# Performance work log

Hardware: AMD Instinct MI355X
Metric: run time of the kernel (lower is better)

Reference implementation:

```python
import jax, jax.numpy as jnp
import numpy as np

N_AE = 512
N_DE = 256
N = 100000
NUM_SEG = 1024
EPS = 1e-5


def setup_inputs() -> dict:
    key = jax.random.key(0)
    ks = jax.random.split(key, 20)
    d_in1 = 2 * N_AE + N_DE  # 1280
    inp = {
        "x": jax.random.normal(ks[0], (N, 2 * N_AE), dtype=jnp.float32),
        "dist_feat": jax.random.normal(ks[1], (N, N_DE), dtype=jnp.float32),
        "atom_idx": jax.random.randint(ks[2], (N,), 0, 100, dtype=jnp.int32),
        "ele_idx": jax.random.randint(ks[3], (N,), 0, NUM_SEG, dtype=jnp.int32),
        # layer 1 params
        "l1_w": jax.random.normal(ks[4], (d_in1, N_AE), dtype=jnp.float32) * (1.0 / np.sqrt(d_in1)),
        "l1_b": jnp.zeros((N_AE,), dtype=jnp.float32),
        "l1_g": jnp.ones((N_AE,), dtype=jnp.float32),
        "l1_be": jnp.zeros((N_AE,), dtype=jnp.float32),
        # layer 2 params (same input width: 2*n_ae + n_de)
        "l2_w": jax.random.normal(ks[5], (d_in1, N_AE), dtype=jnp.float32) * (1.0 / np.sqrt(d_in1)),
        "l2_b": jnp.zeros((N_AE,), dtype=jnp.float32),
        "l2_g": jnp.ones((N_AE,), dtype=jnp.float32),
        "l2_be": jnp.zeros((N_AE,), dtype=jnp.float32),
        # final fc + bn
        "f_w": jax.random.normal(ks[6], (2 * N_AE, N_AE), dtype=jnp.float32) * (1.0 / np.sqrt(2 * N_AE)),
        "f_b": jnp.zeros((N_AE,), dtype=jnp.float32),
        "f_g": jnp.ones((N_AE,), dtype=jnp.float32),
        "f_be": jnp.zeros((N_AE,), dtype=jnp.float32),
    }
    return inp


def _bn(h, gamma, beta):
    # BatchNorm1d in training mode: batch stats, biased variance
    m = jnp.mean(h, axis=0)
    v = jnp.mean(jnp.square(h - m), axis=0)
    return gamma * (h - m) * jax.lax.rsqrt(v + EPS) + beta


def _dist_layer(x_cat, ele_idx, w, b, gamma, beta):
    h = jax.nn.relu(_bn(x_cat @ w + b, gamma, beta))  # [N, n_ae]
    sums = jax.ops.segment_sum(h, ele_idx, num_segments=NUM_SEG)  # [S, n_ae]
    cnt = jax.ops.segment_sum(jnp.ones((h.shape[0],), h.dtype), ele_idx, num_segments=NUM_SEG)
    mean = sums / jnp.maximum(cnt, 1.0)[:, None]
    return jnp.concatenate([h, mean[ele_idx]], axis=1)  # [N, 2*n_ae]


def reference(x, dist_feat, atom_idx, ele_idx,
              l1_w, l1_b, l1_g, l1_be,
              l2_w, l2_b, l2_g, l2_be,
              f_w, f_b, f_g, f_be):
    h = _dist_layer(jnp.concatenate([x, dist_feat], axis=1), ele_idx, l1_w, l1_b, l1_g, l1_be)
    h = _dist_layer(jnp.concatenate([h, dist_feat], axis=1), ele_idx, l2_w, l2_b, l2_g, l2_be)
    out = jax.nn.relu(_bn(h @ f_w + f_b, f_g, f_be))  # [N, n_ae]
    return out
```

## Files before the change

kernel.cpp:

```cpp
#include <hip/hip_runtime.h>
#include <stdint.h>
#include <stdio.h>

#define NOUT 512
#define NSEG 1024

typedef unsigned short u16;
typedef __attribute__((ext_vector_type(4))) float f32x4;
typedef __attribute__((ext_vector_type(8))) short s16x8;
typedef __attribute__((ext_vector_type(4))) unsigned short u16x4;

__device__ __forceinline__ u16 f2b(float f) {
  union { float f; uint32_t u; } v; v.f = f;
  uint32_t r = v.u + 0x7FFFu + ((v.u >> 16) & 1u);
  return (u16)(r >> 16);
}
__device__ __forceinline__ float b2f(u16 b) {
  union { uint32_t u; float f; } v; v.u = ((uint32_t)b) << 16;
  return v.f;
}

typedef __attribute__((address_space(1))) const void GAS;
typedef __attribute__((address_space(3))) void LAS;
__device__ __forceinline__ void llds16(const void* g, void* l) {
  __builtin_amdgcn_global_load_lds((GAS*)g, (LAS*)l, 16, 0, 0);
}

__global__ void k_cast(const float* __restrict__ src, u16* __restrict__ dst, long n4) {
  long i = blockIdx.x * (long)blockDim.x + threadIdx.x;
  long stride = (long)gridDim.x * blockDim.x;
  for (; i < n4; i += stride) {
    float4 v = reinterpret_cast<const float4*>(src)[i];
    u16x4 o;
    o.x = f2b(v.x); o.y = f2b(v.y); o.z = f2b(v.z); o.w = f2b(v.w);
    reinterpret_cast<u16x4*>(dst)[i] = o;
  }
}

__global__ void k_wtcastT(const float* __restrict__ w, u16* __restrict__ out, int K) {
  __shared__ float tile[32][33];
  int k0 = blockIdx.x * 32, c0 = blockIdx.y * 32;
  int t = threadIdx.x;
  int rr = t >> 5, cc = t & 31;
#pragma unroll
  for (int p = 0; p < 4; ++p)
    tile[p * 8 + rr][cc] = w[(long)(k0 + p * 8 + rr) * NOUT + c0 + cc];
  __syncthreads();
#pragma unroll
  for (int p = 0; p < 4; ++p)
    out[(long)(c0 + p * 8 + rr) * K + k0 + cc] = f2b(tile[cc][p * 8 + rr]);
}

__global__ void k_hist(const int* __restrict__ ele, int* __restrict__ cnt, int N) {
  int i = blockIdx.x * blockDim.x + threadIdx.x;
  int stride = gridDim.x * blockDim.x;
  for (; i < N; i += stride) atomicAdd(&cnt[ele[i]], 1);
}

__global__ void k_scan(const int* __restrict__ cnt, int* __restrict__ off) {
  __shared__ int tmp[NSEG];
  int t = threadIdx.x;
  tmp[t] = cnt[t];
  __syncthreads();
  for (int o = 1; o < NSEG; o <<= 1) {
    int add = (t >= o) ? tmp[t - o] : 0;
    __syncthreads();
    tmp[t] += add;
    __syncthreads();
  }
  off[t] = tmp[t] - cnt[t];
}

__global__ void k_scatter(const int* __restrict__ ele, const int* __restrict__ off,
                          int* __restrict__ fill, int* __restrict__ rows, int N) {
  int i = blockIdx.x * blockDim.x + threadIdx.x;
  int stride = gridDim.x * blockDim.x;
  for (; i < N; i += stride) {
    int e = ele[i];
    int p = atomicAdd(&fill[e], 1);
    rows[off[e] + p] = i;
  }
}

__global__ void k_colreduce(const float* __restrict__ ps, const float* __restrict__ pq,
                            float* __restrict__ sum, float* __restrict__ sq, int rows) {
  int gid = blockIdx.x * blockDim.x + threadIdx.x;
  int col = gid & 511;
  int arr = (gid >> 9) & 1;
  int chunk = gid >> 10;
  const float* src = arr ? pq : ps;
  float acc = 0.f;
  for (int r = chunk; r < rows; r += 16) acc += src[(long)r * NOUT + col];
  atomicAdd(arr ? &sq[col] : &sum[col], acc);
}

__global__ void k_finalize(const float* __restrict__ sum, const float* __restrict__ sumsq,
                           const float* __restrict__ g, const float* __restrict__ be,
                           float* __restrict__ A, float* __restrict__ C, int M) {
  int c = threadIdx.x;
  float m = sum[c] / (float)M;
  float v = sumsq[c] / (float)M - m * m;
  float a = g[c] * rsqrtf(v + 1e-5f);
  A[c] = a;
  C[c] = be[c] - a * m;
}

__global__ void k_bnseg(const u16* __restrict__ hp, u16* __restrict__ h, u16* __restrict__ mean,
                        const float* __restrict__ A, const float* __restrict__ C,
                        const int* __restrict__ off, const int* __restrict__ cnt,
                        const int* __restrict__ rows) {
  int s = blockIdx.x;
  int c0 = blockIdx.y * 256 + 2 * threadIdx.x;
  int n = cnt[s], o = off[s];
  float a0 = A[c0], a1 = A[c0 + 1], cc0 = C[c0], cc1 = C[c0 + 1];
  float s0 = 0.f, s1 = 0.f;
  for (int j = 0; j < n; ++j) {
    int r = rows[o + j];
    uint32_t v = *reinterpret_cast<const uint32_t*>(&hp[(long)r * NOUT + c0]);
    float h0 = fmaxf(a0 * b2f((u16)(v & 0xffff)) + cc0, 0.f);
    float h1 = fmaxf(a1 * b2f((u16)(v >> 16)) + cc1, 0.f);
    s0 += h0; s1 += h1;
    *reinterpret_cast<uint32_t*>(&h[(long)r * NOUT + c0]) =
        ((uint32_t)f2b(h1) << 16) | (uint32_t)f2b(h0);
  }
  float inv = 1.f / fmaxf((float)n, 1.f);
  *reinterpret_cast<uint32_t*>(&mean[(long)s * NOUT + c0]) =
      ((uint32_t)f2b(s1 * inv) << 16) | (uint32_t)f2b(s0 * inv);
}

__global__ void k_final(const u16* __restrict__ hp, float* __restrict__ out,
                        const float* __restrict__ A, const float* __restrict__ C, long n4) {
  long i = blockIdx.x * (long)blockDim.x + threadIdx.x;
  long stride = (long)gridDim.x * blockDim.x;
  for (; i < n4; i += stride) {
    u16x4 v = reinterpret_cast<const u16x4*>(hp)[i];
    int c0 = (int)((i * 4) & (NOUT - 1));
    float4 a = *reinterpret_cast<const float4*>(&A[c0]);
    float4 c = *reinterpret_cast<const float4*>(&C[c0]);
    float4 o;
    o.x = fmaxf(a.x * b2f(v.x) + c.x, 0.f);
    o.y = fmaxf(a.y * b2f(v.y) + c.y, 0.f);
    o.z = fmaxf(a.z * b2f(v.z) + c.z, 0.f);
    o.w = fmaxf(a.w * b2f(v.w) + c.w, 0.f);
    reinterpret_cast<float4*>(out)[i] = o;
  }
}

__global__ __launch_bounds__(256, 2) void k_gemm(
    const u16* p0, const u16* p1, int e0, int w0, int w1, int g0, int g1,
    const int* __restrict__ ele,
    const u16* __restrict__ wbt, int ldb, int e0b, int bskip,
    const float* __restrict__ tab, int addtab,
    u16* __restrict__ outp, float* __restrict__ outf, int wf32,
    float* __restrict__ ps, float* __restrict__ pq, int dostats,
    int M, int K) {
  __shared__ __align__(16) u16 As[128 * 32];
  __shared__ __align__(16) u16 Bs[128 * 32];

  int nwg = gridDim.x;
  int bid = blockIdx.x;
  if ((nwg & 7) == 0) {
    int chunk = nwg >> 3;
    bid = (bid & 7) * chunk + (bid >> 3);
  }
  int mt = bid >> 2, ct = bid & 3;
  int brow = mt * 128, bcol = ct * 128;

  int tid = (int)threadIdx.x;
  int lane = tid & 63;
  int wv = tid >> 6;
  int wr = wv >> 1, wc = wv & 1;
  int l4 = lane >> 2;
  int c8 = lane & 3;
  int socl = (c8 ^ ((l4 >> 1) & 3)) * 8;

  int rr0 = brow + wv * 32 + l4;
  int r0 = rr0 < M ? rr0 : M - 1;
  int rr1 = rr0 + 16;
  int r1 = rr1 < M ? rr1 : M - 1;
  int el0 = ele[r0], el1 = ele[r1];

  const u16* a00 = p0 + (long)(g0 ? el0 : r0) * w0 + socl;
  const u16* a01 = p1 + (long)(g1 ? el0 : r0) * w1 + socl - e0;
  const u16* a10 = p0 + (long)(g0 ? el1 : r1) * w0 + socl;
  const u16* a11 = p1 + (long)(g1 ? el1 : r1) * w1 + socl - e0;

  int cb = bcol + wv * 32 + l4;
  const u16* b0p = wbt + (long)cb * ldb + socl;
  const u16* b1p = b0p + (long)16 * ldb;

  u16* ldsA0 = &As[wv * 1024];
  u16* ldsA1 = ldsA0 + 512;
  u16* ldsB0 = &Bs[wv * 1024];
  u16* ldsB1 = ldsB0 + 512;

  f32x4 acc[4][4];
#pragma unroll
  for (int m = 0; m < 4; ++m)
#pragma unroll
    for (int n = 0; n < 4; ++n)
#pragma unroll
      for (int j = 0; j < 4; ++j) acc[m][n][j] = 0.f;

  int l15 = lane & 15, kg = lane >> 4;
  int axr = (kg ^ ((l15 >> 1) & 3)) * 8;
  int KT = K >> 5;
  for (int ks = 0; ks < KT; ++ks) {
    int k0 = ks << 5;
    const u16* sa0 = k0 < e0 ? a00 : a01;
    const u16* sa1 = k0 < e0 ? a10 : a11;
    int bo = k0 + (k0 >= e0b ? bskip : 0);
    __syncthreads();
    llds16(sa0 + k0, ldsA0);
    llds16(sa1 + k0, ldsA1);
    llds16(b0p + bo, ldsB0);
    llds16(b1p + bo, ldsB1);
    __syncthreads();
    s16x8 af[4], bf[4];
#pragma unroll
    for (int m = 0; m < 4; ++m)
      af[m] = *reinterpret_cast<const s16x8*>(&As[(wr * 64 + m * 16 + l15) * 32 + axr]);
#pragma unroll
    for (int n = 0; n < 4; ++n)
      bf[n] = *reinterpret_cast<const s16x8*>(&Bs[(wc * 64 + n * 16 + l15) * 32 + axr]);
#pragma unroll
    for (int m = 0; m < 4; ++m)
#pragma unroll
      for (int n = 0; n < 4; ++n)
        acc[m][n] = __builtin_amdgcn_mfma_f32_16x16x32_bf16(af[m], bf[n], acc[m][n], 0, 0, 0);
  }

  float sums[4] = {0.f, 0.f, 0.f, 0.f}, sqs[4] = {0.f, 0.f, 0.f, 0.f};
#pragma unroll
  for (int m = 0; m < 4; ++m) {
    int row0 = brow + wr * 64 + m * 16 + kg * 4;
#pragma unroll
    for (int n = 0; n < 4; ++n) {
      int col = bcol + wc * 64 + n * 16 + l15;
#pragma unroll
      for (int j = 0; j < 4; ++j) {
        int r = row0 + j;
        if (r < M) {
          float v = acc[m][n][j];
          if (addtab) v += tab[(long)ele[r] * NOUT + col];
          if (wf32) outf[(long)r * NOUT + col] = v;
          else outp[(long)r * NOUT + col] = f2b(v);
          sums[n] += v;
          sqs[n] += v * v;
        }
      }
    }
  }
  if (dostats) {
#pragma unroll
    for (int n = 0; n < 4; ++n) {
      sums[n] += __shfl_xor(sums[n], 16);
      sums[n] += __shfl_xor(sums[n], 32);
      sqs[n] += __shfl_xor(sqs[n], 16);
      sqs[n] += __shfl_xor(sqs[n], 32);
    }
    if (kg == 0) {
      long prow = (long)(mt * 2 + wr) * NOUT;
#pragma unroll
      for (int n = 0; n < 4; ++n) {
        int col = bcol + wc * 64 + n * 16 + l15;
        ps[prow + col] = sums[n];
        pq[prow + col] = sqs[n];
      }
    }
  }
}

extern "C" void kernel_launch(void* const* d_in, const int* in_sizes, int n_in,
                              void* d_out, int out_size, void* d_ws, size_t ws_size,
                              hipStream_t stream) {
  const float* x    = (const float*)d_in[0];
  const float* dist = (const float*)d_in[1];
  const int* ele    = (const int*)d_in[3];
  const float* l1w  = (const float*)d_in[4];
  const float* l1g  = (const float*)d_in[6];
  const float* l1be = (const float*)d_in[7];
  const float* l2w  = (const float*)d_in[8];
  const float* l2g  = (const float*)d_in[10];
  const float* l2be = (const float*)d_in[11];
  const float* fw   = (const float*)d_in[12];
  const float* fg   = (const float*)d_in[14];
  const float* fbe  = (const float*)d_in[15];

  int N = in_sizes[0] / 1024;
  float* out = (float*)d_out;
  u16* xbf = (u16*)d_out;

  int MT = (N + 127) / 128;
  int prows = MT * 2;

  char* w = (char*)d_ws;
  auto alloc = [&](size_t bytes) {
    char* p = w;
    w += (bytes + 255) & ~(size_t)255;
    return p;
  };
  u16* dist_bf = (u16*)alloc((size_t)N * 256 * 2);
  u16* hp      = (u16*)alloc((size_t)N * NOUT * 2);
  u16* h       = (u16*)alloc((size_t)N * NOUT * 2);
  u16* mean    = (u16*)alloc((size_t)NSEG * NOUT * 2);
  u16* w1bt    = (u16*)alloc((size_t)NOUT * 1280 * 2);
  u16* w2bt    = (u16*)alloc((size_t)NOUT * 1280 * 2);
  u16* fbt     = (u16*)alloc((size_t)NOUT * 1024 * 2);
  float* mc2   = (float*)alloc((size_t)NSEG * NOUT * 4);
  float* mc3   = (float*)alloc((size_t)NSEG * NOUT * 4);
  float* ps    = (float*)alloc((size_t)prows * NOUT * 4);
  float* pq    = (float*)alloc((size_t)prows * NOUT * 4);
  float* colsum = (float*)alloc(NOUT * 4 * 2);
  float* colsumsq = colsum + NOUT;
  float* bnA   = (float*)alloc(NOUT * 4);
  float* bnC   = (float*)alloc(NOUT * 4);
  int* seg_cnt = (int*)alloc(NSEG * 4);
  int* seg_off = (int*)alloc(NSEG * 4);
  int* seg_fill = (int*)alloc(NSEG * 4);
  int* rows    = (int*)alloc((size_t)N * 4);

  size_t need = (size_t)(w - (char*)d_ws);
  if (need > ws_size) {
    fprintf(stderr, "kernel_launch: ws too small: need %zu have %zu\n", need, ws_size);
    return;
  }

  long n4x = (long)N * 1024 / 4;
  long n4d = (long)N * 256 / 4;
  long n4h = (long)N * NOUT / 4;
  int gemmGrid = MT * 4;
  int mcGrid = (NSEG / 128) * 4;
  dim3 bnsegGrid(NSEG, 2);

  k_cast<<<4096, 256, 0, stream>>>(x, xbf, n4x);
  k_cast<<<2048, 256, 0, stream>>>(dist, dist_bf, n4d);
  dim3 wt1(1280 / 32, 16), wt3(1024 / 32, 16);
  k_wtcastT<<<wt1, 256, 0, stream>>>(l1w, w1bt, 1280);
  k_wtcastT<<<wt1, 256, 0, stream>>>(l2w, w2bt, 1280);
  k_wtcastT<<<wt3, 256, 0, stream>>>(fw, fbt, 1024);

  hipMemsetAsync(seg_cnt, 0, NSEG * 4, stream);
  hipMemsetAsync(seg_fill, 0, NSEG * 4, stream);
  k_hist<<<512, 256, 0, stream>>>(ele, seg_cnt, N);
  k_scan<<<1, NSEG, 0, stream>>>(seg_cnt, seg_off);
  k_scatter<<<512, 256, 0, stream>>>(ele, seg_off, seg_fill, rows, N);

  k_gemm<<<gemmGrid, 256, 0, stream>>>(xbf, dist_bf, 1024, 1024, 256, 0, 0, ele,
                                       w1bt, 1280, 1280, 0, mc2, 0,
                                       hp, mc2, 0, ps, pq, 1, N, 1280);
  hipMemsetAsync(colsum, 0, NOUT * 4 * 2, stream);
  k_colreduce<<<64, 256, 0, stream>>>(ps, pq, colsum, colsumsq, prows);
  k_finalize<<<1, NOUT, 0, stream>>>(colsum, colsumsq, l1g, l1be, bnA, bnC, N);
  k_bnseg<<<bnsegGrid, 128, 0, stream>>>(hp, h, mean, bnA, bnC, seg_off, seg_cnt, rows);

  k_gemm<<<mcGrid, 256, 0, stream>>>(mean, mean, 512, 512, 512, 0, 0, ele,
                                     w2bt + 512, 1280, 512, 0, mc2, 0,
                                     hp, mc2, 1, ps, pq, 0, NSEG, 512);
  k_gemm<<<gemmGrid, 256, 0, stream>>>(h, dist_bf, 512, 512, 256, 0, 0, ele,
                                       w2bt, 1280, 512, 512, mc2, 1,
                                       hp, mc2, 0, ps, pq, 1, N, 768);
  hipMemsetAsync(colsum, 0, NOUT * 4 * 2, stream);
  k_colreduce<<<64, 256, 0, stream>>>(ps, pq, colsum, colsumsq, prows);
  k_finalize<<<1, NOUT, 0, stream>>>(colsum, colsumsq, l2g, l2be, bnA, bnC, N);
  k_bnseg<<<bnsegGrid, 128, 0, stream>>>(hp, h, mean, bnA, bnC, seg_off, seg_cnt, rows);

  k_gemm<<<mcGrid, 256, 0, stream>>>(mean, mean, 512, 512, 512, 0, 0, ele,
                                     fbt + 512, 1024, 512, 0, mc3, 0,
                                     hp, mc3, 1, ps, pq, 0, NSEG, 512);
  k_gemm<<<gemmGrid, 256, 0, stream>>>(h, h, 512, 512, 512, 0, 0, ele,
                                       fbt, 1024, 512, 0, mc3, 1,
                                       hp, mc3, 0, ps, pq, 1, N, 512);
  hipMemsetAsync(colsum, 0, NOUT * 4 * 2, stream);
  k_colreduce<<<64, 256, 0, stream>>>(ps, pq, colsum, colsumsq, prows);
  k_finalize<<<1, NOUT, 0, stream>>>(colsum, colsumsq, fg, fbe, bnA, bnC, N);
  k_final<<<4096, 256, 0, stream>>>(hp, out, bnA, bnC, n4h);
}
```

Measured before the change: 1.112 ms.

## Enlarge GEMM tile to 128x256xK64 and fuse BN column stats via atomics

The GEMM tile grows from 128x128 with K=32 to 128x256 with K=64, so each wave holds 4x8 MFMA accumulators. This raises operand reuse per LDS load and halves the number of barriers per K. The XCD block remapping is generalized to grids that are not a multiple of 8. Per-tile partial BN statistics are now atomically added straight into column sums, which drops the partial-sum buffers and the separate colreduce kernel. In exchange it uses more registers and LDS, which may lower occupancy, and it adds atomic contention and nondeterministic float summation order.

```diff
diff --git a/kernel.cpp b/kernel.cpp
--- a/kernel.cpp
+++ b/kernel.cpp
@@ -80,18 +80,6 @@
     int p = atomicAdd(&fill[e], 1);
     rows[off[e] + p] = i;
   }
-}
-
-__global__ void k_colreduce(const float* __restrict__ ps, const float* __restrict__ pq,
-                            float* __restrict__ sum, float* __restrict__ sq, int rows) {
-  int gid = blockIdx.x * blockDim.x + threadIdx.x;
-  int col = gid & 511;
-  int arr = (gid >> 9) & 1;
-  int chunk = gid >> 10;
-  const float* src = arr ? pq : ps;
-  float acc = 0.f;
-  for (int r = chunk; r < rows; r += 16) acc += src[(long)r * NOUT + col];
-  atomicAdd(arr ? &sq[col] : &sum[col], acc);
 }
 
 __global__ void k_finalize(const float* __restrict__ sum, const float* __restrict__ sumsq,
@@ -152,99 +140,111 @@
     const u16* __restrict__ wbt, int ldb, int e0b, int bskip,
     const float* __restrict__ tab, int addtab,
     u16* __restrict__ outp, float* __restrict__ outf, int wf32,
-    float* __restrict__ ps, float* __restrict__ pq, int dostats,
+    float* __restrict__ csum, float* __restrict__ csq, int dostats,
     int M, int K) {
-  __shared__ __align__(16) u16 As[128 * 32];
-  __shared__ __align__(16) u16 Bs[128 * 32];
+  __shared__ __align__(16) u16 As[128 * 64];
+  __shared__ __align__(16) u16 Bs[256 * 64];
 
   int nwg = gridDim.x;
-  int bid = blockIdx.x;
-  if ((nwg & 7) == 0) {
-    int chunk = nwg >> 3;
-    bid = (bid & 7) * chunk + (bid >> 3);
-  }
-  int mt = bid >> 2, ct = bid & 3;
-  int brow = mt * 128, bcol = ct * 128;
+  int orig = blockIdx.x;
+  int q = nwg >> 3, r8 = nwg & 7;
+  int xcd = orig & 7, loc = orig >> 3;
+  int bid = (xcd < r8 ? xcd * (q + 1) : r8 * (q + 1) + (xcd - r8) * q) + loc;
+  int mt = bid >> 1, ct = bid & 1;
+  int brow = mt * 128, bcol = ct * 256;
 
   int tid = (int)threadIdx.x;
   int lane = tid & 63;
-  int wv = tid >> 6;
-  int wr = wv >> 1, wc = wv & 1;
-  int l4 = lane >> 2;
-  int c8 = lane & 3;
-  int socl = (c8 ^ ((l4 >> 1) & 3)) * 8;
-
-  int rr0 = brow + wv * 32 + l4;
-  int r0 = rr0 < M ? rr0 : M - 1;
-  int rr1 = rr0 + 16;
-  int r1 = rr1 < M ? rr1 : M - 1;
-  int el0 = ele[r0], el1 = ele[r1];
-
-  const u16* a00 = p0 + (long)(g0 ? el0 : r0) * w0 + socl;
-  const u16* a01 = p1 + (long)(g1 ? el0 : r0) * w1 + socl - e0;
-  const u16* a10 = p0 + (long)(g0 ? el1 : r1) * w0 + socl;
-  const u16* a11 = p1 + (long)(g1 ? el1 : r1) * w1 + socl - e0;
-
-  int cb = bcol + wv * 32 + l4;
-  const u16* b0p = wbt + (long)cb * ldb + socl;
-  const u16* b1p = b0p + (long)16 * ldb;
-
-  u16* ldsA0 = &As[wv * 1024];
-  u16* ldsA1 = ldsA0 + 512;
-  u16* ldsB0 = &Bs[wv * 1024];
-  u16* ldsB1 = ldsB0 + 512;
-
-  f32x4 acc[4][4];
+  int wid = tid >> 6;
+  int wr = wid >> 1, wc = wid & 1;
+  int l15 = lane & 15, kg = lane >> 4;
+
+  int rl = tid >> 3;
+  int soct = ((tid & 7) ^ (rl & 7)) * 8;
+
+  int rida0[4], rida1[4];
+#pragma unroll
+  for (int c = 0; c < 4; ++c) {
+    int gr = brow + rl + 32 * c;
+    if (gr >= M) gr = M - 1;
+    int e = (g0 | g1) ? ele[gr] : 0;
+    rida0[c] = g0 ? e : gr;
+    rida1[c] = g1 ? e : gr;
+  }
+  const u16* bptr[8];
+#pragma unroll
+  for (int c = 0; c < 8; ++c)
+    bptr[c] = wbt + (long)(bcol + rl + 32 * c) * ldb + soct;
+
+  int ch0 = (kg ^ (l15 & 7)) * 8;
+  int ch1 = ((4 | kg) ^ (l15 & 7)) * 8;
+  int arow = (wr * 64 + l15) * 64;
+  int brow_l = (wc * 128 + l15) * 64;
+
+  f32x4 acc[4][8];
 #pragma unroll
   for (int m = 0; m < 4; ++m)
 #pragma unroll
-    for (int n = 0; n < 4; ++n)
+    for (int n = 0; n < 8; ++n)
 #pragma unroll
       for (int j = 0; j < 4; ++j) acc[m][n][j] = 0.f;
 
-  int l15 = lane & 15, kg = lane >> 4;
-  int axr = (kg ^ ((l15 >> 1) & 3)) * 8;
-  int KT = K >> 5;
-  for (int ks = 0; ks < KT; ++ks) {
-    int k0 = ks << 5;
-    const u16* sa0 = k0 < e0 ? a00 : a01;
-    const u16* sa1 = k0 < e0 ? a10 : a11;
+  int KT = K >> 6;
+  for (int t = 0; t < KT; ++t) {
+    int k0 = t << 6;
+    __syncthreads();
+    if (k0 < e0) {
+#pragma unroll
+      for (int c = 0; c < 4; ++c)
+        llds16(p0 + (long)rida0[c] * w0 + soct + k0, &As[c * 2048 + wid * 512]);
+    } else {
+      int ko = k0 - e0;
+#pragma unroll
+      for (int c = 0; c < 4; ++c)
+        llds16(p1 + (long)rida1[c] * w1 + soct + ko, &As[c * 2048 + wid * 512]);
+    }
     int bo = k0 + (k0 >= e0b ? bskip : 0);
+#pragma unroll
+    for (int c = 0; c < 8; ++c)
+      llds16(bptr[c] + bo, &Bs[c * 2048 + wid * 512]);
     __syncthreads();
-    llds16(sa0 + k0, ldsA0);
-    llds16(sa1 + k0, ldsA1);
-    llds16(b0p + bo, ldsB0);
-    llds16(b1p + bo, ldsB1);
-    __syncthreads();
-    s16x8 af[4], bf[4];
-#pragma unroll
-    for (int m = 0; m < 4; ++m)
-      af[m] = *reinterpret_cast<const s16x8*>(&As[(wr * 64 + m * 16 + l15) * 32 + axr]);
-#pragma unroll
-    for (int n = 0; n < 4; ++n)
-      bf[n] = *reinterpret_cast<const s16x8*>(&Bs[(wc * 64 + n * 16 + l15) * 32 + axr]);
-#pragma unroll
-    for (int m = 0; m < 4; ++m)
-#pragma unroll
-      for (int n = 0; n < 4; ++n)
-        acc[m][n] = __builtin_amdgcn_mfma_f32_16x16x32_bf16(af[m], bf[n], acc[m][n], 0, 0, 0);
-  }
-
-  float sums[4] = {0.f, 0.f, 0.f, 0.f}, sqs[4] = {0.f, 0.f, 0.f, 0.f};
+#pragma unroll
+    for (int kk = 0; kk < 2; ++kk) {
+      int ch = kk ? ch1 : ch0;
+      s16x8 af[4], bf[8];
+#pragma unroll
+      for (int m = 0; m < 4; ++m)
+        af[m] = *reinterpret_cast<const s16x8*>(&As[arow + m * 1024 + ch]);
+#pragma unroll
+      for (int n = 0; n < 8; ++n)
+        bf[n] = *reinterpret_cast<const s16x8*>(&Bs[brow_l + n * 1024 + ch]);
+#pragma unroll
+      for (int m = 0; m < 4; ++m)
+#pragma unroll
+        for (int n = 0; n < 8; ++n)
+          acc[m][n] = __builtin_amdgcn_mfma_f32_16x16x32_bf16(af[m], bf[n], acc[m][n], 0, 0, 0);
+    }
+  }
+
+  float sums[8], sqs[8];
+#pragma unroll
+  for (int n = 0; n < 8; ++n) { sums[n] = 0.f; sqs[n] = 0.f; }
 #pragma unroll
   for (int m = 0; m < 4; ++m) {
     int row0 = brow + wr * 64 + m * 16 + kg * 4;
 #pragma unroll
-    for (int n = 0; n < 4; ++n) {
-      int col = bcol + wc * 64 + n * 16 + l15;
-#pragma unroll
-      for (int j = 0; j < 4; ++j) {
-        int r = row0 + j;
-        if (r < M) {
+    for (int j = 0; j < 4; ++j) {
+      int r = row0 + j;
+      if (r < M) {
+        long rb = (long)r * NOUT;
+        long tb = addtab ? (long)ele[r] * NOUT : 0;
+#pragma unroll
+        for (int n = 0; n < 8; ++n) {
+          int col = bcol + wc * 128 + n * 16 + l15;
           float v = acc[m][n][j];
-          if (addtab) v += tab[(long)ele[r] * NOUT + col];
-          if (wf32) outf[(long)r * NOUT + col] = v;
-          else outp[(long)r * NOUT + col] = f2b(v);
+          if (addtab) v += tab[tb + col];
+          if (wf32) outf[rb + col] = v;
+          else outp[rb + col] = f2b(v);
           sums[n] += v;
           sqs[n] += v * v;
         }
@@ -253,19 +253,18 @@
   }
   if (dostats) {
 #pragma unroll
-    for (int n = 0; n < 4; ++n) {
+    for (int n = 0; n < 8; ++n) {
       sums[n] += __shfl_xor(sums[n], 16);
       sums[n] += __shfl_xor(sums[n], 32);
       sqs[n] += __shfl_xor(sqs[n], 16);
       sqs[n] += __shfl_xor(sqs[n], 32);
     }
     if (kg == 0) {
-      long prow = (long)(mt * 2 + wr) * NOUT;
-#pragma unroll
-      for (int n = 0; n < 4; ++n) {
-        int col = bcol + wc * 64 + n * 16 + l15;
-        ps[prow + col] = sums[n];
-        pq[prow + col] = sqs[n];
+#pragma unroll
+      for (int n = 0; n < 8; ++n) {
+        int col = bcol + wc * 128 + n * 16 + l15;
+        atomicAdd(&csum[col], sums[n]);
+        atomicAdd(&csq[col], sqs[n]);
       }
     }
   }
@@ -292,7 +291,6 @@
   u16* xbf = (u16*)d_out;
 
   int MT = (N + 127) / 128;
-  int prows = MT * 2;
 
   char* w = (char*)d_ws;
   auto alloc = [&](size_t bytes) {
@@ -309,8 +307,6 @@
   u16* fbt     = (u16*)alloc((size_t)NOUT * 1024 * 2);
   float* mc2   = (float*)alloc((size_t)NSEG * NOUT * 4);
   float* mc3   = (float*)alloc((size_t)NSEG * NOUT * 4);
-  float* ps    = (float*)alloc((size_t)prows * NOUT * 4);
-  float* pq    = (float*)alloc((size_t)prows * NOUT * 4);
   float* colsum = (float*)alloc(NOUT * 4 * 2);
   float* colsumsq = colsum + NOUT;
   float* bnA   = (float*)alloc(NOUT * 4);
@@ -329,8 +325,8 @@
   long n4x = (long)N * 1024 / 4;
   long n4d = (long)N * 256 / 4;
   long n4h = (long)N * NOUT / 4;
-  int gemmGrid = MT * 4;
-  int mcGrid = (NSEG / 128) * 4;
+  int gemmGrid = MT * 2;
+  int mcGrid = (NSEG / 128) * 2;
   dim3 bnsegGrid(NSEG, 2);
 
   k_cast<<<4096, 256, 0, stream>>>(x, xbf, n4x);
@@ -346,33 +342,30 @@
   k_scan<<<1, NSEG, 0, stream>>>(seg_cnt, seg_off);
   k_scatter<<<512, 256, 0, stream>>>(ele, seg_off, seg_fill, rows, N);
 
+  hipMemsetAsync(colsum, 0, NOUT * 4 * 2, stream);
   k_gemm<<<gemmGrid, 256, 0, stream>>>(xbf, dist_bf, 1024, 1024, 256, 0, 0, ele,
                                        w1bt, 1280, 1280, 0, mc2, 0,
-                                       hp, mc2, 0, ps, pq, 1, N, 1280);
-  hipMemsetAsync(colsum, 0, NOUT * 4 * 2, stream);
-  k_colreduce<<<64, 256, 0, stream>>>(ps, pq, colsum, colsumsq, prows);
+                                       hp, mc2, 0, colsum, colsumsq, 1, N, 1280);
   k_finalize<<<1, NOUT, 0, stream>>>(colsum, colsumsq, l1g, l1be, bnA, bnC, N);
   k_bnseg<<<bnsegGrid, 128, 0, stream>>>(hp, h, mean, bnA, bnC, seg_off, seg_cnt, rows);
 
   k_gemm<<<mcGrid, 256, 0, stream>>>(mean, mean, 512, 512, 512, 0, 0, ele,
                                      w2bt + 512, 1280, 512, 0, mc2, 0,
-                                     hp, mc2, 1, ps, pq, 0, NSEG, 512);
+                                     hp, mc2, 1, colsum, colsumsq, 0, NSEG, 512);
+  hipMemsetAsync(colsum, 0, NOUT * 4 * 2, stream);
   k_gemm<<<gemmGrid, 256, 0, stream>>>(h, dist_bf, 512, 512, 256, 0, 0, ele,
                                        w2bt, 1280, 512, 512, mc2, 1,
-                                       hp, mc2, 0, ps, pq, 1, N, 768);
-  hipMemsetAsync(colsum, 0, NOUT * 4 * 2, stream);
-  k_colreduce<<<64, 256, 0, stream>>>(ps, pq, colsum, colsumsq, prows);
+                                       hp, mc2, 0, colsum, colsumsq, 1, N, 768);
   k_finalize<<<1, NOUT, 0, stream>>>(colsum, colsumsq, l2g, l2be, bnA, bnC, N);
   k_bnseg<<<bnsegGrid, 128, 0, stream>>>(hp, h, mean, bnA, bnC, seg_off, seg_cnt, rows);
 
   k_gemm<<<mcGrid, 256, 0, stream>>>(mean, mean, 512, 512, 512, 0, 0, ele,
                                      fbt + 512, 1024, 512, 0, mc3, 0,
-                                     hp, mc3, 1, ps, pq, 0, NSEG, 512);
+                                     hp, mc3, 1, colsum, colsumsq, 0, NSEG, 512);
+  hipMemsetAsync(colsum, 0, NOUT * 4 * 2, stream);
   k_gemm<<<gemmGrid, 256, 0, stream>>>(h, h, 512, 512, 512, 0, 0, ele,
                                        fbt, 1024, 512, 0, mc3, 1,
-                                       hp, mc3, 0, ps, pq, 1, N, 512);
-  hipMemsetAsync(colsum, 0, NOUT * 4 * 2, stream);
-  k_colreduce<<<64, 256, 0, stream>>>(ps, pq, colsum, colsumsq, prows);
+                                       hp, mc3, 0, colsum, colsumsq, 1, N, 512);
   k_finalize<<<1, NOUT, 0, stream>>>(colsum, colsumsq, fg, fbe, bnA, bnC, N);
   k_final<<<4096, 256, 0, stream>>>(hp, out, bnA, bnC, n4h);
 }
```

Result: no change. 1.107 ms (-0.4%).
